# Optimization experiments

Hardware: AMD Instinct MI355X
Metric: run time of the kernel (lower is better)

Reference implementation:

```python
import jax, jax.numpy as jnp
import numpy as np

NUM_PTS = 8   # num_points_per_face
K = 5         # self.k


def _sq_dist(x, y):
    # squared euclidean distance matrix (Nx, Ny); matches torch.cdist**2 / sum((a-b)**2)
    x2 = jnp.sum(x * x, axis=1)[:, None]
    y2 = jnp.sum(y * y, axis=1)[None, :]
    d = x2 + y2 - 2.0 * (x @ y.T)
    return jnp.maximum(d, 0.0)


def setup_inputs() -> dict:
    key = jax.random.key(0)
    k1, k2, k3, k4, k5, k6, k7 = jax.random.split(key, 7)
    V, Fs, Ft = 2048, 4096, 4096
    return {
        "source_vertices": jax.random.normal(k1, (1, V, 3), dtype=jnp.float32),
        "source_faces": jax.random.randint(k2, (Fs, 3), 0, V),
        "target_vertices": jax.random.normal(k3, (1, V, 3), dtype=jnp.float32),
        "target_faces": jax.random.randint(k4, (3, Ft), 0, V),
        "face_probs": jax.random.uniform(k5, (Fs,), dtype=jnp.float32),
        "r1u": jax.random.uniform(k6, (Fs, NUM_PTS), dtype=jnp.float32),
        "r2u": jax.random.uniform(k7, (Fs, NUM_PTS), dtype=jnp.float32),
    }


def reference(source_vertices, source_faces, target_vertices, target_faces, face_probs, r1u, r2u):
    sv = source_vertices[0]                 # (V, 3)
    tv = target_vertices[0]                 # (V, 3)
    tf = target_faces.T                     # (Ft, 3)
    Fs = source_faces.shape[0]

    src_bc = sv[source_faces].mean(axis=1)  # (Fs, 3) source barycenters
    tgt_bc = tv[tf].mean(axis=1)            # (Ft, 3) target barycenters

    # ---- forward loss: prob-weighted min squared distance to target barycenters
    d_fwd = _sq_dist(src_bc, tgt_bc)        # (Fs, Ft)
    forward_loss = jnp.sum(face_probs * jnp.min(d_fwd, axis=1))

    # ---- sample points from triangles via barycentric coords
    r1 = jnp.sqrt(r1u)
    w1 = 1.0 - r1
    w2 = r1 * (1.0 - r2u)
    w3 = r1 * r2u
    v1 = sv[source_faces[:, 0]]             # (Fs, 3)
    v2 = sv[source_faces[:, 1]]
    v3 = sv[source_faces[:, 2]]
    pts = (w1[..., None] * v1[:, None] + w2[..., None] * v2[:, None]
           + w3[..., None] * v3[:, None]).reshape(-1, 3)   # (P, 3), P = Fs*NUM_PTS
    pt_faces = jnp.repeat(jnp.arange(Fs), NUM_PTS)          # (P,)
    pt_probs = face_probs[pt_faces]                         # (P,)

    # ---- reverse loss, batched over all P points
    d_src = _sq_dist(pts, src_bc)                           # (P, Fs)
    neg_d, idx = jax.lax.top_k(-d_src, K + 1)               # K+1 smallest distances
    tri_dists = -neg_d                                      # (P, K+1)
    mask = idx != pt_faces[:, None]                         # exclude own face
    has_self = jnp.any(~mask, axis=1)
    excl_pos = jnp.where(has_self, jnp.argmin(mask, axis=1), K + 1)  # (P,)
    t = jnp.arange(K)
    sel = t[None, :] + (t[None, :] >= excl_pos[:, None]).astype(jnp.int32)  # (P, K)
    valid_dists = jnp.take_along_axis(tri_dists, sel, axis=1)   # (P, K)
    valid_idx = jnp.take_along_axis(idx, sel, axis=1)           # (P, K)
    valid_probs = face_probs[valid_idx]                         # (P, K)

    min_tgt = jnp.min(_sq_dist(pts, tgt_bc), axis=1)            # (P,)

    reverse_loss = jnp.sum(pt_probs * min_tgt
                           + (1.0 - pt_probs) * jnp.mean(valid_probs * valid_dists, axis=1))
    return forward_loss + reverse_loss
```

## Files before the change

kernel.cpp:

```cpp
#include <hip/hip_runtime.h>
#include <math.h>

#define FS 4096
#define FT 4096
#define TS 512
#define NPH 8
#define BIGF 3.0e38f
#define KEYINF 0xFFFFFFFFu

typedef float v2f __attribute__((ext_vector_type(2)));

__device__ __forceinline__ unsigned umin32(unsigned a, unsigned b) { return a < b ? a : b; }
__device__ __forceinline__ unsigned umax32(unsigned a, unsigned b) { return a < b ? b : a; }

__device__ __forceinline__ unsigned med3u(unsigned a, unsigned b, unsigned c) {
    unsigned d;
    asm("v_med3_u32 %0, %1, %2, %3" : "=v"(d) : "v"(a), "v"(b), "v"(c));
    return d;
}

__device__ __forceinline__ v2f pk_fma(v2f a, v2f b, v2f c) {
    v2f d;
    asm("v_pk_fma_f32 %0, %1, %2, %3" : "=v"(d) : "v"(a), "v"(b), "v"(c));
    return d;
}
__device__ __forceinline__ v2f pk_add(v2f a, v2f b) {
    v2f d;
    asm("v_pk_add_f32 %0, %1, %2" : "=v"(d) : "v"(a), "v"(b));
    return d;
}

__device__ __forceinline__ void gl_lds16(const float4* g, float4* l) {
    __builtin_amdgcn_global_load_lds(
        (__attribute__((address_space(1))) void*)(g),
        (__attribute__((address_space(3))) void*)(l), 16, 0, 0);
}

__device__ __forceinline__ float block_reduce_sum(float v) {
    __shared__ float s[8];
    for (int o = 32; o > 0; o >>= 1) v += __shfl_down(v, o, 64);
    int lane = threadIdx.x & 63, wid = threadIdx.x >> 6;
    if (lane == 0) s[wid] = v;
    __syncthreads();
    int nw = blockDim.x >> 6;
    v = (threadIdx.x < (unsigned)nw) ? s[threadIdx.x] : 0.f;
    if (wid == 0)
        for (int o = 4; o > 0; o >>= 1) v += __shfl_down(v, o, 64);
    return v;
}

#define CE(x, y) { unsigned _n = umin32(x, y); y = umax32(x, y); x = _n; }

__device__ __forceinline__ void merge32(unsigned s[6]) {
    #pragma unroll
    for (int m = 1; m <= 16; m <<= 1) {
        unsigned b0 = __shfl_xor(s[0], m, 64), b1 = __shfl_xor(s[1], m, 64);
        unsigned b2 = __shfl_xor(s[2], m, 64), b3 = __shfl_xor(s[3], m, 64);
        unsigned b4 = __shfl_xor(s[4], m, 64), b5 = __shfl_xor(s[5], m, 64);
        unsigned l0 = s[0], l1 = s[1];
        unsigned l2 = umin32(s[2], b5), l3 = umin32(s[3], b4);
        unsigned l4 = umin32(s[4], b3), l5 = umin32(s[5], b2);
        unsigned l6 = b1, l7 = b0;
        CE(l0, l4) CE(l1, l5) CE(l2, l6) CE(l3, l7)
        CE(l0, l2) CE(l1, l3) CE(l4, l6) CE(l5, l7)
        CE(l0, l1) CE(l2, l3) CE(l4, l5) CE(l6, l7)
        s[0] = l0; s[1] = l1; s[2] = l2; s[3] = l3; s[4] = l4; s[5] = l5;
    }
}

__global__ __launch_bounds__(64) void k_prep(
        const float* __restrict__ sv, const int* __restrict__ sf,
        const float* __restrict__ tv, const int* __restrict__ tf,
        float4* __restrict__ sbc2, float4* __restrict__ tbc2,
        float4* __restrict__ sbcr, float* __restrict__ out) {
    int i = blockIdx.x * 64 + threadIdx.x;
    if (i == 0) out[0] = 0.f;
    if (i >= FS) return;
    const float third = 1.f / 3.f;
    int a = sf[3*i], b = sf[3*i+1], c = sf[3*i+2];
    float x = (sv[3*a  ] + sv[3*b  ] + sv[3*c  ]) * third;
    float y = (sv[3*a+1] + sv[3*b+1] + sv[3*c+1]) * third;
    float z = (sv[3*a+2] + sv[3*b+2] + sv[3*c+2]) * third;
    float n2 = x*x + y*y + z*z;
    sbcr[i] = make_float4(x, y, z, n2);
    int ta = tf[i], tb = tf[FT + i], tc = tf[2*FT + i];
    float tx = (tv[3*ta  ] + tv[3*tb  ] + tv[3*tc  ]) * third;
    float ty = (tv[3*ta+1] + tv[3*tb+1] + tv[3*tc+1]) * third;
    float tz = (tv[3*ta+2] + tv[3*tb+2] + tv[3*tc+2]) * third;
    float tn2 = tx*tx + ty*ty + tz*tz;

    int tt = i >> 10, cc = i & 1023;
    int g = cc >> 6, half = (cc >> 5) & 1, pp = cc & 31;
    int lo4 = tt*1024 + g*32 + pp, hi4 = lo4 + 512;
    float* S = (float*)sbc2;
    S[4*lo4 + half]     = -2.f*x;  S[4*lo4 + 2 + half] = -2.f*y;
    S[4*hi4 + half]     = -2.f*z;  S[4*hi4 + 2 + half] = n2;
    float* T = (float*)tbc2;
    T[4*lo4 + half]     = -2.f*tx; T[4*lo4 + 2 + half] = -2.f*ty;
    T[4*hi4 + half]     = -2.f*tz; T[4*hi4 + 2 + half] = tn2;
}

__global__ __launch_bounds__(256, 4) void k_main(
        const float* __restrict__ sv, const int* __restrict__ sf,
        const float* __restrict__ fp,
        const float* __restrict__ r1u, const float* __restrict__ r2u,
        const float4* __restrict__ sbc2, const float4* __restrict__ tbc2,
        const float4* __restrict__ sbcr, float* __restrict__ out) {
    __shared__ float4 tileS[TS];
    __shared__ float4 tileT[TS];
    int tid  = threadIdx.x;
    int seg  = tid & 31;
    int slot = tid >> 5;
    float contrib = 0.f;

    if (blockIdx.x < 1024) {
        int pt0  = blockIdx.x * 32 + slot * 4;
        int face = pt0 >> 3;

        int a = sf[3*face], b = sf[3*face+1], c = sf[3*face+2];
        float ax = sv[3*a], ay = sv[3*a+1], az = sv[3*a+2];
        float bx = sv[3*b], by = sv[3*b+1], bz = sv[3*b+2];
        float cx = sv[3*c], cy = sv[3*c+1], cz = sv[3*c+2];
        float4 r14 = ((const float4*)r1u)[pt0 >> 2];
        float4 r24 = ((const float4*)r2u)[pt0 >> 2];
        v2f pxb[4], pyb[4], pzb[4], p2b[4];
        {
            float r1a[4] = {r14.x, r14.y, r14.z, r14.w};
            float r2a[4] = {r24.x, r24.y, r24.z, r24.w};
            #pragma unroll
            for (int i = 0; i < 4; ++i) {
                float r1 = sqrtf(r1a[i]);
                float w1 = 1.f - r1, w2 = r1 * (1.f - r2a[i]), w3 = r1 * r2a[i];
                float px = w1*ax + w2*bx + w3*cx;
                float py = w1*ay + w2*by + w3*cy;
                float pz = w1*az + w2*bz + w3*cz;
                float p2 = px*px + py*py + pz*pz;
                pxb[i] = (v2f){px, px}; pyb[i] = (v2f){py, py};
                pzb[i] = (v2f){pz, pz}; p2b[i] = (v2f){p2, p2};
            }
        }

        unsigned s0[4], s1[4], s2[4];
        #pragma unroll
        for (int i = 0; i < 4; ++i) { s0[i]=KEYINF; s1[i]=KEYINF; s2[i]=KEYINF; }
        v2f vm2[4];
        #pragma unroll
        for (int i = 0; i < 4; ++i) vm2[i] = (v2f){BIGF, BIGF};

        for (int p = 0; p < NPH; ++p) {
            int loB = ((p >> 1) << 10) + ((p & 1) << 8);
            __syncthreads();
            gl_lds16(&sbc2[loB + tid],       &tileS[tid]);
            gl_lds16(&sbc2[loB + 512 + tid], &tileS[256 + tid]);
            gl_lds16(&tbc2[loB + tid],       &tileT[tid]);
            gl_lds16(&tbc2[loB + 512 + tid], &tileT[256 + tid]);
            __syncthreads();
            unsigned jja = (unsigned)(p * TS + seg);
            #pragma unroll 4
            for (int jp = 0; jp < 8; ++jp) {
                float4 lo = tileS[(jp << 5) + seg];
                float4 hi = tileS[256 + (jp << 5) + seg];
                v2f cx2 = {lo.x, lo.y}, cy2 = {lo.z, lo.w};
                v2f cz2 = {hi.x, hi.y}, cw2 = {hi.z, hi.w};
                #pragma unroll
                for (int i = 0; i < 4; ++i) {
                    v2f d2 = pk_add(cw2, p2b[i]);
                    d2 = pk_fma(pzb[i], cz2, d2);
                    d2 = pk_fma(pyb[i], cy2, d2);
                    d2 = pk_fma(pxb[i], cx2, d2);
                    unsigned ka = (__float_as_uint(d2.x) & 0xFFFFF000u) | jja;
                    unsigned kb = (__float_as_uint(d2.y) & 0xFFFFF000u) | (jja + 32u);
                    unsigned n0 = umin32(s0[i], ka);
                    unsigned n1 = med3u(s0[i], s1[i], ka);
                    unsigned n2 = med3u(s1[i], s2[i], ka);
                    s0[i]=n0; s1[i]=n1; s2[i]=n2;
                    n0 = umin32(s0[i], kb);
                    n1 = med3u(s0[i], s1[i], kb);
                    n2 = med3u(s1[i], s2[i], kb);
                    s0[i]=n0; s1[i]=n1; s2[i]=n2;
                }
                jja += 64;
            }
            #pragma unroll 4
            for (int jp = 0; jp < 8; ++jp) {
                float4 lo = tileT[(jp << 5) + seg];
                float4 hi = tileT[256 + (jp << 5) + seg];
                v2f cx2 = {lo.x, lo.y}, cy2 = {lo.z, lo.w};
                v2f cz2 = {hi.x, hi.y}, cw2 = {hi.z, hi.w};
                #pragma unroll
                for (int i = 0; i < 4; ++i) {
                    v2f t = pk_fma(pzb[i], cz2, cw2);
                    t = pk_fma(pyb[i], cy2, t);
                    t = pk_fma(pxb[i], cx2, t);
                    vm2[i].x = fminf(vm2[i].x, t.x);
                    vm2[i].y = fminf(vm2[i].y, t.y);
                }
            }
        }

        float vm[4];
        #pragma unroll
        for (int i = 0; i < 4; ++i) {
            float v = fminf(vm2[i].x, vm2[i].y);
            v = fminf(v, __shfl_xor(v, 1, 64));
            v = fminf(v, __shfl_xor(v, 2, 64));
            v = fminf(v, __shfl_xor(v, 4, 64));
            v = fminf(v, __shfl_xor(v, 8, 64));
            v = fminf(v, __shfl_xor(v, 16, 64));
            vm[i] = v;
        }

        float pf = fp[face];
        float csum = 0.f;
        #pragma unroll
        for (int i = 0; i < 4; ++i) {
            unsigned srt[6] = {s0[i], s1[i], s2[i], KEYINF, KEYINF, KEYINF};
            merge32(srt);
            if (seg == 0) {
                int   q0 = srt[0] & 0xFFF, q1 = srt[1] & 0xFFF, q2 = srt[2] & 0xFFF;
                int   q3 = srt[3] & 0xFFF, q4 = srt[4] & 0xFFF, q5 = srt[5] & 0xFFF;
                float d0 = __uint_as_float(srt[0] & 0xFFFFF000u);
                float d1 = __uint_as_float(srt[1] & 0xFFFFF000u);
                float d2 = __uint_as_float(srt[2] & 0xFFFFF000u);
                float d3 = __uint_as_float(srt[3] & 0xFFFFF000u);
                float d4 = __uint_as_float(srt[4] & 0xFFFFF000u);
                float d5 = __uint_as_float(srt[5] & 0xFFFFF000u);

                int skip = 5;
                if      (q0 == face) skip = 0;
                else if (q1 == face) skip = 1;
                else if (q2 == face) skip = 2;
                else if (q3 == face) skip = 3;
                else if (q4 == face) skip = 4;

                float s = 0.f;
                if (skip != 0) s += fp[q0] * d0;
                if (skip != 1) s += fp[q1] * d1;
                if (skip != 2) s += fp[q2] * d2;
                if (skip != 3) s += fp[q3] * d3;
                if (skip != 4) s += fp[q4] * d4;
                if (skip != 5) s += fp[q5] * d5;

                float mtd = fmaxf(vm[i] + p2b[i].x, 0.f);
                csum += pf * mtd + (1.f - pf) * (s * 0.2f);
            }
        }
        if (seg == 0) contrib = csum;
    } else {
        int f0 = (blockIdx.x - 1024) * 32 + slot * 4;
        float qw[4];
        v2f qxb[4], qyb[4], qzb[4];
        #pragma unroll
        for (int i = 0; i < 4; ++i) {
            float4 q = sbcr[f0 + i];
            qxb[i] = (v2f){q.x, q.x}; qyb[i] = (v2f){q.y, q.y};
            qzb[i] = (v2f){q.z, q.z}; qw[i] = q.w;
        }
        v2f vf2[4];
        #pragma unroll
        for (int i = 0; i < 4; ++i) vf2[i] = (v2f){BIGF, BIGF};

        for (int p = 0; p < NPH; ++p) {
            int loB = ((p >> 1) << 10) + ((p & 1) << 8);
            __syncthreads();
            gl_lds16(&tbc2[loB + tid],       &tileT[tid]);
            gl_lds16(&tbc2[loB + 512 + tid], &tileT[256 + tid]);
            __syncthreads();
            #pragma unroll 4
            for (int jp = 0; jp < 8; ++jp) {
                float4 lo = tileT[(jp << 5) + seg];
                float4 hi = tileT[256 + (jp << 5) + seg];
                v2f cx2 = {lo.x, lo.y}, cy2 = {lo.z, lo.w};
                v2f cz2 = {hi.x, hi.y}, cw2 = {hi.z, hi.w};
                #pragma unroll
                for (int i = 0; i < 4; ++i) {
                    v2f t = pk_fma(qzb[i], cz2, cw2);
                    t = pk_fma(qyb[i], cy2, t);
                    t = pk_fma(qxb[i], cx2, t);
                    vf2[i].x = fminf(vf2[i].x, t.x);
                    vf2[i].y = fminf(vf2[i].y, t.y);
                }
            }
        }
        float vf[4];
        #pragma unroll
        for (int i = 0; i < 4; ++i) {
            float v = fminf(vf2[i].x, vf2[i].y);
            v = fminf(v, __shfl_xor(v, 1, 64));
            v = fminf(v, __shfl_xor(v, 2, 64));
            v = fminf(v, __shfl_xor(v, 4, 64));
            v = fminf(v, __shfl_xor(v, 8, 64));
            v = fminf(v, __shfl_xor(v, 16, 64));
            vf[i] = v;
        }
        if (seg == 0)
            contrib = fp[f0  ] * fmaxf(vf[0] + qw[0], 0.f)
                    + fp[f0+1] * fmaxf(vf[1] + qw[1], 0.f)
                    + fp[f0+2] * fmaxf(vf[2] + qw[2], 0.f)
                    + fp[f0+3] * fmaxf(vf[3] + qw[3], 0.f);
    }

    float tot = block_reduce_sum(contrib);
    if (tid == 0) atomicAdd(out, tot);
}

extern "C" void kernel_launch(void* const* d_in, const int* in_sizes, int n_in,
                              void* d_out, int out_size, void* d_ws, size_t ws_size,
                              hipStream_t stream) {
    const float* sv  = (const float*)d_in[0];
    const int*   sf  = (const int*)  d_in[1];
    const float* tv  = (const float*)d_in[2];
    const int*   tf  = (const int*)  d_in[3];
    const float* fp  = (const float*)d_in[4];
    const float* r1u = (const float*)d_in[5];
    const float* r2u = (const float*)d_in[6];
    float* out = (float*)d_out;

    char* ws = (char*)d_ws;
    float4* sbc2 = (float4*)(ws);
    float4* tbc2 = (float4*)(ws + 65536);
    float4* sbcr = (float4*)(ws + 131072);

    k_prep<<<64,   64,  0, stream>>>(sv, sf, tv, tf, sbc2, tbc2, sbcr, out);
    k_main<<<1152, 256, 0, stream>>>(sv, sf, fp, r1u, r2u, sbc2, tbc2, sbcr, out);
}
```

Baseline: 112.6 us.

## Double-buffer LDS tiles so prefetch overlaps compute with one barrier per phase

The tile is halved to 256 entries and the loop runs over 16 phases. Shared tiles become ping-pong buffers, so the next phase's global-to-LDS load is issued before computing on the current buffer. This removes one of the two barriers per phase and hides load latency behind the distance math. Tagging the sort keys now uses a single v_and_or_b32, and the packed FMAs accumulate in place, to trim instruction count. The cost is twice as many loop iterations and barriers, plus reliance on the barrier waiting for the async LDS loads.

```diff
diff --git a/kernel.cpp b/kernel.cpp
--- a/kernel.cpp
+++ b/kernel.cpp
@@ -3,8 +3,8 @@
 
 #define FS 4096
 #define FT 4096
-#define TS 512
-#define NPH 8
+#define TS 256
+#define NPH 16
 #define BIGF 3.0e38f
 #define KEYINF 0xFFFFFFFFu
 
@@ -19,15 +19,24 @@
     return d;
 }
 
+__device__ __forceinline__ unsigned and_or(unsigned a, unsigned m, unsigned o) {
+    unsigned d;
+    asm("v_and_or_b32 %0, %1, %2, %3" : "=v"(d) : "v"(a), "v"(m), "v"(o));
+    return d;
+}
+
+__device__ __forceinline__ v2f pk_add(v2f a, v2f b) {
+    v2f d;
+    asm("v_pk_add_f32 %0, %1, %2" : "=v"(d) : "v"(a), "v"(b));
+    return d;
+}
 __device__ __forceinline__ v2f pk_fma(v2f a, v2f b, v2f c) {
     v2f d;
     asm("v_pk_fma_f32 %0, %1, %2, %3" : "=v"(d) : "v"(a), "v"(b), "v"(c));
     return d;
 }
-__device__ __forceinline__ v2f pk_add(v2f a, v2f b) {
-    v2f d;
-    asm("v_pk_add_f32 %0, %1, %2" : "=v"(d) : "v"(a), "v"(b));
-    return d;
+__device__ __forceinline__ void pk_fma_acc(v2f& d, v2f a, v2f b) {
+    asm("v_pk_fma_f32 %0, %1, %2, %0" : "+v"(d) : "v"(a), "v"(b));
 }
 
 __device__ __forceinline__ void gl_lds16(const float4* g, float4* l) {
@@ -100,14 +109,16 @@
     T[4*hi4 + half]     = -2.f*tz; T[4*hi4 + 2 + half] = tn2;
 }
 
+#define STAGE_OFF(p) ((((p) >> 2) << 10) + (((p) & 3) << 7) + (tid & 127) + ((tid >> 7) << 9))
+
 __global__ __launch_bounds__(256, 4) void k_main(
         const float* __restrict__ sv, const int* __restrict__ sf,
         const float* __restrict__ fp,
         const float* __restrict__ r1u, const float* __restrict__ r2u,
         const float4* __restrict__ sbc2, const float4* __restrict__ tbc2,
         const float4* __restrict__ sbcr, float* __restrict__ out) {
-    __shared__ float4 tileS[TS];
-    __shared__ float4 tileT[TS];
+    __shared__ float4 tileS[2][TS];
+    __shared__ float4 tileT[2][TS];
     int tid  = threadIdx.x;
     int seg  = tid & 31;
     int slot = tid >> 5;
@@ -147,29 +158,37 @@
         #pragma unroll
         for (int i = 0; i < 4; ++i) vm2[i] = (v2f){BIGF, BIGF};
 
+        unsigned kMask = 0xFFFFF000u;
+
+        {
+            int off = STAGE_OFF(0);
+            gl_lds16(&sbc2[off], &tileS[0][tid]);
+            gl_lds16(&tbc2[off], &tileT[0][tid]);
+        }
+
         for (int p = 0; p < NPH; ++p) {
-            int loB = ((p >> 1) << 10) + ((p & 1) << 8);
+            int buf = p & 1;
             __syncthreads();
-            gl_lds16(&sbc2[loB + tid],       &tileS[tid]);
-            gl_lds16(&sbc2[loB + 512 + tid], &tileS[256 + tid]);
-            gl_lds16(&tbc2[loB + tid],       &tileT[tid]);
-            gl_lds16(&tbc2[loB + 512 + tid], &tileT[256 + tid]);
-            __syncthreads();
+            if (p + 1 < NPH) {
+                int off = STAGE_OFF(p + 1);
+                gl_lds16(&sbc2[off], &tileS[buf ^ 1][tid]);
+                gl_lds16(&tbc2[off], &tileT[buf ^ 1][tid]);
+            }
             unsigned jja = (unsigned)(p * TS + seg);
-            #pragma unroll 4
-            for (int jp = 0; jp < 8; ++jp) {
-                float4 lo = tileS[(jp << 5) + seg];
-                float4 hi = tileS[256 + (jp << 5) + seg];
+            #pragma unroll
+            for (int jp = 0; jp < 4; ++jp) {
+                float4 lo = tileS[buf][(jp << 5) + seg];
+                float4 hi = tileS[buf][128 + (jp << 5) + seg];
                 v2f cx2 = {lo.x, lo.y}, cy2 = {lo.z, lo.w};
                 v2f cz2 = {hi.x, hi.y}, cw2 = {hi.z, hi.w};
                 #pragma unroll
                 for (int i = 0; i < 4; ++i) {
                     v2f d2 = pk_add(cw2, p2b[i]);
-                    d2 = pk_fma(pzb[i], cz2, d2);
-                    d2 = pk_fma(pyb[i], cy2, d2);
-                    d2 = pk_fma(pxb[i], cx2, d2);
-                    unsigned ka = (__float_as_uint(d2.x) & 0xFFFFF000u) | jja;
-                    unsigned kb = (__float_as_uint(d2.y) & 0xFFFFF000u) | (jja + 32u);
+                    pk_fma_acc(d2, pzb[i], cz2);
+                    pk_fma_acc(d2, pyb[i], cy2);
+                    pk_fma_acc(d2, pxb[i], cx2);
+                    unsigned ka = and_or(__float_as_uint(d2.x), kMask, jja);
+                    unsigned kb = and_or(__float_as_uint(d2.y), kMask, jja + 32u);
                     unsigned n0 = umin32(s0[i], ka);
                     unsigned n1 = med3u(s0[i], s1[i], ka);
                     unsigned n2 = med3u(s1[i], s2[i], ka);
@@ -181,17 +200,17 @@
                 }
                 jja += 64;
             }
-            #pragma unroll 4
-            for (int jp = 0; jp < 8; ++jp) {
-                float4 lo = tileT[(jp << 5) + seg];
-                float4 hi = tileT[256 + (jp << 5) + seg];
+            #pragma unroll
+            for (int jp = 0; jp < 4; ++jp) {
+                float4 lo = tileT[buf][(jp << 5) + seg];
+                float4 hi = tileT[buf][128 + (jp << 5) + seg];
                 v2f cx2 = {lo.x, lo.y}, cy2 = {lo.z, lo.w};
                 v2f cz2 = {hi.x, hi.y}, cw2 = {hi.z, hi.w};
                 #pragma unroll
                 for (int i = 0; i < 4; ++i) {
                     v2f t = pk_fma(pzb[i], cz2, cw2);
-                    t = pk_fma(pyb[i], cy2, t);
-                    t = pk_fma(pxb[i], cx2, t);
+                    pk_fma_acc(t, pyb[i], cy2);
+                    pk_fma_acc(t, pxb[i], cx2);
                     vm2[i].x = fminf(vm2[i].x, t.x);
                     vm2[i].y = fminf(vm2[i].y, t.y);
                 }
@@ -260,23 +279,28 @@
         #pragma unroll
         for (int i = 0; i < 4; ++i) vf2[i] = (v2f){BIGF, BIGF};
 
+        {
+            int off = STAGE_OFF(0);
+            gl_lds16(&tbc2[off], &tileT[0][tid]);
+        }
         for (int p = 0; p < NPH; ++p) {
-            int loB = ((p >> 1) << 10) + ((p & 1) << 8);
+            int buf = p & 1;
             __syncthreads();
-            gl_lds16(&tbc2[loB + tid],       &tileT[tid]);
-            gl_lds16(&tbc2[loB + 512 + tid], &tileT[256 + tid]);
-            __syncthreads();
-            #pragma unroll 4
-            for (int jp = 0; jp < 8; ++jp) {
-                float4 lo = tileT[(jp << 5) + seg];
-                float4 hi = tileT[256 + (jp << 5) + seg];
+            if (p + 1 < NPH) {
+                int off = STAGE_OFF(p + 1);
+                gl_lds16(&tbc2[off], &tileT[buf ^ 1][tid]);
+            }
+            #pragma unroll
+            for (int jp = 0; jp < 4; ++jp) {
+                float4 lo = tileT[buf][(jp << 5) + seg];
+                float4 hi = tileT[buf][128 + (jp << 5) + seg];
                 v2f cx2 = {lo.x, lo.y}, cy2 = {lo.z, lo.w};
                 v2f cz2 = {hi.x, hi.y}, cw2 = {hi.z, hi.w};
                 #pragma unroll
                 for (int i = 0; i < 4; ++i) {
                     v2f t = pk_fma(qzb[i], cz2, cw2);
-                    t = pk_fma(qyb[i], cy2, t);
-                    t = pk_fma(qxb[i], cx2, t);
+                    pk_fma_acc(t, qyb[i], cy2);
+                    pk_fma_acc(t, qxb[i], cx2);
                     vf2[i].x = fminf(vf2[i].x, t.x);
                     vf2[i].y = fminf(vf2[i].y, t.y);
                 }
```

After: 114.8 us. Within noise of the previous version (+1.9%).
